# Optimization experiments

Hardware: AMD Instinct MI355X
Metric: run time of the kernel (lower is better)

Reference implementation:

```python
import jax, jax.numpy as jnp
import numpy as np

N, X_DIM, Z_DIM, H = 4096, 256, 128, 512
NUM_ACTIONS = 4
TEMPERATURE = 0.1


def _init_linear(key, fan_in, fan_out):
    kw, kb = jax.random.split(key)
    bound = 1.0 / np.sqrt(fan_in)
    W = jax.random.uniform(kw, (fan_in, fan_out), minval=-bound, maxval=bound, dtype=jnp.float32)
    b = jax.random.uniform(kb, (fan_out,), minval=-bound, maxval=bound, dtype=jnp.float32)
    return W, b


def setup_inputs() -> dict:
    key = jax.random.key(0)
    ks = jax.random.split(key, 9)
    s = jax.random.normal(ks[0], (N, X_DIM), dtype=jnp.float32)
    sp = jax.random.normal(ks[1], (N, X_DIM), dtype=jnp.float32)
    a = jax.random.randint(ks[2], (N,), 0, NUM_ACTIONS)
    a1h = jax.nn.one_hot(a, NUM_ACTIONS, dtype=jnp.float32)
    # phi: x_dim -> 512 -> 512 -> z_dim
    pW0, pb0 = _init_linear(ks[3], X_DIM, H)
    pW1, pb1 = _init_linear(ks[4], H, H)
    pW2, pb2 = _init_linear(ks[5], H, Z_DIM)
    # g: x_dim + 4 -> 512 -> 512 -> z_dim
    gW0, gb0 = _init_linear(ks[6], X_DIM + NUM_ACTIONS, H)
    gW1, gb1 = _init_linear(ks[7], H, H)
    gW2, gb2 = _init_linear(ks[8], H, Z_DIM)
    return {"s": s, "sp": sp, "a1h": a1h,
            "pW0": pW0, "pb0": pb0, "pW1": pW1, "pb1": pb1, "pW2": pW2, "pb2": pb2,
            "gW0": gW0, "gb0": gb0, "gW1": gW1, "gb1": gb1, "gW2": gW2, "gb2": gb2}


def _mlp(x, W0, b0, W1, b1, W2, b2):
    h = jax.nn.relu(x @ W0 + b0)
    h = jax.nn.relu(h @ W1 + b1)
    return h @ W2 + b2


def reference(s, sp, a1h, pW0, pb0, pW1, pb1, pW2, pb2, gW0, gb0, gW1, gb1, gW2, gb2):
    z = _mlp(s, pW0, pb0, pW1, pb1, pW2, pb2)                      # [N, D]
    zpos = _mlp(jnp.concatenate([sp, a1h], axis=-1), gW0, gb0, gW1, gb1, gW2, gb2)  # [N, D]
    # -||z_i - zpos_j||^2 / T via the GEMM trick (avoids the [N,N,D] diff tensor)
    sq_z = jnp.sum(z * z, axis=-1, keepdims=True)                  # [N, 1]
    sq_p = jnp.sum(zpos * zpos, axis=-1)                            # [N]
    logits = -(sq_z + sq_p[None, :] - 2.0 * z @ zpos.T) / TEMPERATURE  # [N, N]
    # cross-entropy with targets = arange(N): diagonal is the positive
    log_probs = jax.nn.log_softmax(logits, axis=-1)
    loss = -jnp.mean(jnp.diagonal(log_probs))
    return loss
```

## Files before the change

kernel.cpp:

```cpp
#include <hip/hip_runtime.h>
#include <math.h>

#define NR 4096
#define HD 512
#define NJR 16
#define INV_T 10.0f

typedef __attribute__((ext_vector_type(8))) short bf16x8;
typedef __attribute__((ext_vector_type(4))) short short4v;
typedef __attribute__((ext_vector_type(4))) float f32x4;

typedef const unsigned int __attribute__((address_space(1)))* gas_t;
typedef unsigned int __attribute__((address_space(3)))* las_t;

__device__ __forceinline__ unsigned short f2bf(float f) {
  union { float f; unsigned u; } v; v.f = f;
  unsigned r = v.u + 0x7fff + ((v.u >> 16) & 1);
  return (unsigned short)(r >> 16);
}
__device__ __forceinline__ float bf2f(unsigned short b) {
  union { unsigned u; float f; } v; v.u = ((unsigned)b) << 16;
  return v.f;
}


__device__ __forceinline__ void wt_unit(int local, int tid, const float* W,
                                        unsigned short* Wt, int N, int ksh) {
  const int idx8 = tid & 127;
  const int h = idx8 & 1, p = idx8 >> 1, hi = p >> 4, l15 = p & 15;
  int s0 = local * 2 + (tid >> 7);
  int rf = s0 >> ksh, ks = s0 & ((1 << ksh) - 1);
  int n = rf * 16 + l15, k0 = ks * 32 + hi * 4 + h * 16;
  short4v o = { (short)f2bf(W[(size_t)(k0 + 0) * N + n]),
                (short)f2bf(W[(size_t)(k0 + 1) * N + n]),
                (short)f2bf(W[(size_t)(k0 + 2) * N + n]),
                (short)f2bf(W[(size_t)(k0 + 3) * N + n]) };
  *(short4v*)((char*)Wt + (size_t)s0 * 1024 + idx8 * 8) = o;
}

__global__ __launch_bounds__(256) void prep(
    const float* __restrict__ s, const float* __restrict__ sp,
    const float* __restrict__ a1h,
    unsigned short* __restrict__ Sb, unsigned short* __restrict__ SPb,
    int* __restrict__ aidx, float* __restrict__ sqp,
    const float* __restrict__ pW0, unsigned short* __restrict__ pW0t,
    const float* __restrict__ gW0, unsigned short* __restrict__ gW0t,
    float* __restrict__ out) {
  const int tid = threadIdx.x;
  for (int u = blockIdx.x; u < 2320; u += 580) {
    if (u < 16) {
      int r = u * 256 + tid;
      int a = 0;
#pragma unroll
      for (int j = 0; j < 4; ++j) if (a1h[(size_t)r * 4 + j] > 0.5f) a = j;
      aidx[r] = a;
      sqp[r] = 0.f;
      if (u == 0 && tid == 0) out[0] = 0.f;
      continue;
    }
    if (u < 2064) {
      const int b = u;
      const float* src = (b < 1040) ? s : sp;
      unsigned short* dst = (b < 1040) ? Sb : SPb;
      int lb = (b < 1040) ? b - 16 : b - 1040;
      const int idx8 = tid & 127;
      const int h = idx8 & 1, p = idx8 >> 1, hi = p >> 4, l15 = p & 15;
      int s0 = lb * 2 + (tid >> 7);
      int rf = s0 >> 3, ks = s0 & 7;
      int row = rf * 16 + l15, c0 = ks * 32 + hi * 4 + h * 16;
      float4 v = *(const float4*)&src[(size_t)row * 256 + c0];
      short4v o = { (short)f2bf(v.x), (short)f2bf(v.y), (short)f2bf(v.z), (short)f2bf(v.w) };
      *(short4v*)((char*)dst + (size_t)s0 * 1024 + idx8 * 8) = o;
      continue;
    }
    int local = u - 2064;
    if (local < 128) wt_unit(local, tid, pW0, pW0t, 512, 3);
    else             wt_unit(local - 128, tid, gW0, gW0t, 512, 3);
  }
}

template <int BM, int K, bool RELU, bool GB, bool SQ, bool RIDERS>
__global__ __launch_bounds__(256) void gemm_p3(
    const unsigned short* __restrict__ A0, const unsigned short* __restrict__ A1,
    const unsigned short* __restrict__ W0, const unsigned short* __restrict__ W1,
    const float* __restrict__ b0, const float* __restrict__ b1,
    unsigned short* __restrict__ C0, unsigned short* __restrict__ C1,
    float* __restrict__ sqp, int N, int gx, int gy,
    const int* __restrict__ aidx, const float* __restrict__ gW0f,
    const float* __restrict__ rpW1, unsigned short* __restrict__ rpW1t,
    const float* __restrict__ rpW2, unsigned short* __restrict__ rpW2t,
    const float* __restrict__ rgW1, unsigned short* __restrict__ rgW1t,
    const float* __restrict__ rgW2, unsigned short* __restrict__ rgW2t) {
  const int tid = threadIdx.x;
  const int ngemm = gx * gy * 2;
  if (RIDERS && (int)blockIdx.x >= ngemm) {
    int local = blockIdx.x - ngemm;
    if (local < 256)      wt_unit(local, tid, rpW1, rpW1t, 512, 4);
    else if (local < 320) wt_unit(local - 256, tid, rpW2, rpW2t, 128, 4);
    else if (local < 576) wt_unit(local - 320, tid, rgW1, rgW1t, 512, 4);
    else                  wt_unit(local - 576, tid, rgW2, rgW2t, 128, 4);
    return;
  }
  constexpr int KS = K >> 5;
  constexpr int NSTEP = K >> 6;
  constexpr int ABYTES = BM * 128;
  constexpr int BBYTES = 8192;
  constexpr int NA = BM >> 5;
  constexpr int WM_FR = BM >> 5;
  constexpr int V = NA + 2;
  __shared__ char lds[3 * (ABYTES + BBYTES)];
  char* AsB = lds;
  char* BsB = lds + 3 * ABYTES;

  const int bid = blockIdx.x;
  const int bx = bid % gx, by = (bid / gx) % gy, z = bid / (gx * gy);
  const int lane = tid & 63, w = tid >> 6;
  const int wm = w >> 1, wn = w & 1;
  const char* Ab = (const char*)(z ? A1 : A0);
  const char* Wb = (const char*)(z ? W1 : W0);
  const float* bias = z ? b1 : b0;
  char* Cb = (char*)(z ? C1 : C0);
  const int bm = bx * BM, bn = by * 64;
  const int lane16 = lane * 16;

  auto stage = [&](int buf, int st) {
#pragma unroll
    for (int u = 0; u < NA; ++u) {
      const int sl = w * NA + u;
      const char* src = Ab + ((size_t)((bm >> 4) + (sl >> 1)) * KS + st * 2 + (sl & 1)) * 1024 + lane16;
      __builtin_amdgcn_global_load_lds((gas_t)src, (las_t)(AsB + buf * ABYTES + sl * 1024), 16, 0, 0);
    }
#pragma unroll
    for (int u = 0; u < 2; ++u) {
      const int sl = w * 2 + u;
      const char* src = Wb + ((size_t)((bn >> 4) + (sl >> 1)) * KS + st * 2 + (sl & 1)) * 1024 + lane16;
      __builtin_amdgcn_global_load_lds((gas_t)src, (las_t)(BsB + buf * BBYTES + sl * 1024), 16, 0, 0);
    }
  };

  f32x4 acc[WM_FR][2] = {};
  stage(0, 0);
  stage(1, 1);
#pragma unroll
  for (int st = 0; st < NSTEP; ++st) {
    const int buf = st % 3;
    if (st + 2 < NSTEP) {
      stage((st + 2) % 3, st + 2);
      if constexpr (V == 6) asm volatile("s_waitcnt vmcnt(12)" ::: "memory");
      else                  asm volatile("s_waitcnt vmcnt(8)" ::: "memory");
    } else if (st + 1 < NSTEP) {
      if constexpr (V == 6) asm volatile("s_waitcnt vmcnt(6)" ::: "memory");
      else                  asm volatile("s_waitcnt vmcnt(4)" ::: "memory");
    } else {
      asm volatile("s_waitcnt vmcnt(0)" ::: "memory");
    }
    __builtin_amdgcn_s_barrier();
#pragma unroll
    for (int kss = 0; kss < 2; ++kss) {
      bf16x8 af[WM_FR], bfv[2];
#pragma unroll
      for (int i = 0; i < WM_FR; ++i)
        af[i] = *(const bf16x8*)(AsB + buf * ABYTES + ((wm * WM_FR + i) * 2 + kss) * 1024 + lane16);
#pragma unroll
      for (int j = 0; j < 2; ++j)
        bfv[j] = *(const bf16x8*)(BsB + buf * BBYTES + ((wn * 2 + j) * 2 + kss) * 1024 + lane16);
#pragma unroll
      for (int i = 0; i < WM_FR; ++i)
#pragma unroll
        for (int j = 0; j < 2; ++j)
          acc[i][j] = __builtin_amdgcn_mfma_f32_16x16x32_bf16(bfv[j], af[i], acc[i][j], 0, 0, 0);
    }
    __builtin_amdgcn_s_barrier();
  }

  const int l15 = lane & 15, hi = lane >> 4;
  const int NS = N >> 5;
  const int row0 = bm + wm * (BM / 2);
  const int col0 = bn + wn * 32;
  float sq[WM_FR];
  int ar[WM_FR];
#pragma unroll
  for (int i = 0; i < WM_FR; ++i) { sq[i] = 0.f; ar[i] = 0; }
  if (GB && z == 1) {
#pragma unroll
    for (int i = 0; i < WM_FR; ++i) ar[i] = aidx[row0 + i * 16 + l15];
  }
  float4 bi0 = *(const float4*)&bias[col0 + hi * 4];
  float4 bi1 = *(const float4*)&bias[col0 + 16 + hi * 4];
#pragma unroll
  for (int i = 0; i < WM_FR; ++i) {
    const int rfC = (row0 >> 4) + i;
    float v[8] = { acc[i][0][0] + bi0.x, acc[i][0][1] + bi0.y,
                   acc[i][0][2] + bi0.z, acc[i][0][3] + bi0.w,
                   acc[i][1][0] + bi1.x, acc[i][1][1] + bi1.y,
                   acc[i][1][2] + bi1.z, acc[i][1][3] + bi1.w };
    if (GB && z == 1) {
      float4 g0 = *(const float4*)&gW0f[(size_t)(256 + ar[i]) * N + col0 + hi * 4];
      float4 g1 = *(const float4*)&gW0f[(size_t)(256 + ar[i]) * N + col0 + 16 + hi * 4];
      v[0] += g0.x; v[1] += g0.y; v[2] += g0.z; v[3] += g0.w;
      v[4] += g1.x; v[5] += g1.y; v[6] += g1.z; v[7] += g1.w;
    }
    bf16x8 r;
#pragma unroll
    for (int t = 0; t < 8; ++t) {
      float vv = RELU ? fmaxf(v[t], 0.f) : v[t];
      unsigned short cv = f2bf(vv);
      r[t] = (short)cv;
      if (SQ) { float vb = bf2f(cv); sq[i] += vb * vb; }
    }
    *(bf16x8*)(Cb + (size_t)(rfC * NS + (col0 >> 5)) * 1024 + lane16) = r;
  }
  if (SQ && z == 1) {
#pragma unroll
    for (int i = 0; i < WM_FR; ++i) {
      float t = sq[i];
      t += __shfl_xor(t, 16, 64);
      t += __shfl_xor(t, 32, 64);
      if (lane < 16) atomicAdd(&sqp[row0 + i * 16 + lane], t);
    }
  }
}

__global__ __launch_bounds__(256) void logits_fm(
    const unsigned short* __restrict__ Zb, const unsigned short* __restrict__ Zpb,
    const float* __restrict__ sqp, float* __restrict__ wm_,
    float* __restrict__ wsum, float* __restrict__ wdiag) {
  const int tid = threadIdx.x, lane = tid & 63, w = tid >> 6;
  const int l15 = lane & 15, hi = lane >> 4;
  const int i0 = blockIdx.x * 128, jr = blockIdx.y;
  const int row32 = i0 + w * 32;
  const int jbase = jr * 256;
  const int lane16 = lane * 16;
  const char* Zc = (const char*)Zb;
  const char* Pc = (const char*)Zpb;

  bf16x8 afr[2][4];
#pragma unroll
  for (int rf = 0; rf < 2; ++rf)
#pragma unroll
    for (int ks = 0; ks < 4; ++ks)
      afr[rf][ks] = *(const bf16x8*)(Zc + (size_t)(((row32 >> 4) + rf) * 4 + ks) * 1024 + lane16);

  float m[2] = {-INFINITY, -INFINITY}, sv[2] = {0.f, 0.f}, dd[2] = {0.f, 0.f};
  bool hasd[2] = {false, false};
  const int grow0 = row32 + l15, grow1 = row32 + 16 + l15;

#pragma unroll
  for (int g = 0; g < 4; ++g) {
    f32x4 acc[2][4] = {};
#pragma unroll
    for (int ks = 0; ks < 4; ++ks)
#pragma unroll
      for (int q = 0; q < 4; ++q) {
        bf16x8 bfv = *(const bf16x8*)(Pc + (size_t)(((jbase >> 4) + g * 4 + q) * 4 + ks) * 1024 + lane16);
        acc[0][q] = __builtin_amdgcn_mfma_f32_16x16x32_bf16(bfv, afr[0][ks], acc[0][q], 0, 0, 0);
        acc[1][q] = __builtin_amdgcn_mfma_f32_16x16x32_bf16(bfv, afr[1][ks], acc[1][q], 0, 0, 0);
      }
    f32x4 spq[4];
#pragma unroll
    for (int q = 0; q < 4; ++q)
      spq[q] = *(const f32x4*)&sqp[jbase + (g * 4 + q) * 16 + hi * 4];
#pragma unroll
    for (int rf = 0; rf < 2; ++rf) {
      const int grow = rf ? grow1 : grow0;
      float lv[16];
      float lmax = -INFINITY;
#pragma unroll
      for (int q = 0; q < 4; ++q)
#pragma unroll
        for (int e = 0; e < 4; ++e) {
          const int j = jbase + (g * 4 + q) * 16 + hi * 4 + e;
          float x = (2.f * acc[rf][q][e] - spq[q][e]) * INV_T;
          lv[q * 4 + e] = x;
          lmax = fmaxf(lmax, x);
          if (j == grow) { dd[rf] = x; hasd[rf] = true; }
        }
      float mn = fmaxf(m[rf], lmax);
      float sc = __expf(m[rf] - mn);
      float ls = 0.f;
#pragma unroll
      for (int t = 0; t < 16; ++t) ls += __expf(lv[t] - mn);
      sv[rf] = sv[rf] * sc + ls;
      m[rf] = mn;
    }
  }

#pragma unroll
  for (int rf = 0; rf < 2; ++rf) {
    const int grow = rf ? grow1 : grow0;
    float mm = m[rf], ss = sv[rf];
#pragma unroll
    for (int off = 16; off <= 32; off <<= 1) {
      float mo = __shfl_xor(mm, off, 64);
      float so = __shfl_xor(ss, off, 64);
      float mn = fmaxf(mm, mo);
      ss = ss * __expf(mm - mn) + so * __expf(mo - mn);
      mm = mn;
    }
    if (hi == 0) {
      wm_[(size_t)jr * NR + grow] = mm;
      wsum[(size_t)jr * NR + grow] = ss;
    }
    if (hasd[rf]) wdiag[grow] = dd[rf];
  }
}

__global__ __launch_bounds__(256) void finalize(const float* __restrict__ wm,
    const float* __restrict__ wsum, const float* __restrict__ wdiag,
    float* __restrict__ out) {
  int r = blockIdx.x * 256 + threadIdx.x;
  float mm = wm[r];
  float ss = wsum[r];
#pragma unroll
  for (int p = 1; p < NJR; ++p) {
    float mo = wm[(size_t)p * NR + r];
    float so = wsum[(size_t)p * NR + r];
    float mn = fmaxf(mm, mo);
    ss = ss * __expf(mm - mn) + so * __expf(mo - mn);
    mm = mn;
  }
  float loss_r = mm + logf(ss) - wdiag[r];
  float v = loss_r;
#pragma unroll
  for (int off = 32; off; off >>= 1) v += __shfl_xor(v, off, 64);
  __shared__ float partial[4];
  if ((threadIdx.x & 63) == 0) partial[threadIdx.x >> 6] = v;
  __syncthreads();
  if (threadIdx.x == 0)
    atomicAdd(out, (partial[0] + partial[1] + partial[2] + partial[3]) * (1.0f / (float)NR));
}

extern "C" void kernel_launch(void* const* d_in, const int* in_sizes, int n_in,
                              void* d_out, int out_size, void* d_ws, size_t ws_size,
                              hipStream_t stream) {
  const float* s   = (const float*)d_in[0];
  const float* sp  = (const float*)d_in[1];
  const float* a1h = (const float*)d_in[2];
  const float* pW0 = (const float*)d_in[3];
  const float* pb0 = (const float*)d_in[4];
  const float* pW1 = (const float*)d_in[5];
  const float* pb1 = (const float*)d_in[6];
  const float* pW2 = (const float*)d_in[7];
  const float* pb2 = (const float*)d_in[8];
  const float* gW0 = (const float*)d_in[9];
  const float* gb0 = (const float*)d_in[10];
  const float* gW1 = (const float*)d_in[11];
  const float* gb1 = (const float*)d_in[12];
  const float* gW2 = (const float*)d_in[13];
  const float* gb2 = (const float*)d_in[14];

  char* p = (char*)d_ws;
  unsigned short* Sb   = (unsigned short*)p; p += (size_t)NR * 256 * 2;
  unsigned short* SPb  = (unsigned short*)p; p += (size_t)NR * 256 * 2;
  unsigned short* H1   = (unsigned short*)p; p += (size_t)2 * NR * HD * 2;
  unsigned short* H2   = (unsigned short*)p; p += (size_t)2 * NR * HD * 2;
  unsigned short* Zall = (unsigned short*)p; p += (size_t)2 * NR * 128 * 2;
  unsigned short* pW0t = (unsigned short*)p; p += (size_t)256 * 512 * 2;
  unsigned short* pW1t = (unsigned short*)p; p += (size_t)512 * 512 * 2;
  unsigned short* pW2t = (unsigned short*)p; p += (size_t)512 * 128 * 2;
  unsigned short* gW0t = (unsigned short*)p; p += (size_t)256 * 512 * 2;
  unsigned short* gW1t = (unsigned short*)p; p += (size_t)512 * 512 * 2;
  unsigned short* gW2t = (unsigned short*)p; p += (size_t)512 * 128 * 2;
  float* sqp  = (float*)p; p += (size_t)NR * 4;
  float* wm   = (float*)p; p += (size_t)NJR * NR * 4;
  float* wsm  = (float*)p; p += (size_t)NJR * NR * 4;
  float* wdg  = (float*)p; p += (size_t)NR * 4;
  int*   aidx = (int*)p;  p += (size_t)NR * 4;

  unsigned short* H1g = H1 + (size_t)NR * HD;
  unsigned short* H2g = H2 + (size_t)NR * HD;
  unsigned short* Zb  = Zall;
  unsigned short* Zpb = Zall + (size_t)NR * 128;

  dim3 blk(256);
  prep<<<580, blk, 0, stream>>>(s, sp, a1h, Sb, SPb, aidx, sqp,
                                pW0, pW0t, gW0, gW0t, (float*)d_out);

  gemm_p3<128, 256, true, true, false, true><<<1152, blk, 0, stream>>>(
      Sb, SPb, pW0t, gW0t, pb0, gb0, H1, H1g, nullptr, 512, 32, 8, aidx, gW0,
      pW1, pW1t, pW2, pW2t, gW1, gW1t, gW2, gW2t);

  gemm_p3<128, 512, true, false, false, false><<<512, blk, 0, stream>>>(
      H1, H1g, pW1t, gW1t, pb1, gb1, H2, H2g, nullptr, 512, 32, 8, nullptr, nullptr,
      nullptr, nullptr, nullptr, nullptr, nullptr, nullptr, nullptr, nullptr);

  gemm_p3<64, 512, false, false, true, false><<<256, blk, 0, stream>>>(
      H2, H2g, pW2t, gW2t, pb2, gb2, Zb, Zpb, sqp, 128, 64, 2, nullptr, nullptr,
      nullptr, nullptr, nullptr, nullptr, nullptr, nullptr, nullptr, nullptr);

  logits_fm<<<dim3(32, NJR), blk, 0, stream>>>(Zb, Zpb, sqp, wm, wsm, wdg);
  finalize<<<NR / 256, blk, 0, stream>>>(wm, wsm, wdg, (float*)d_out);
}
```

Baseline: 46.18 us.

## Double-buffer zpos tiles in LDS and compute softmax in base-2 domain

New measurement: 47.87 us. 3.7% more time.

```diff
diff --git a/kernel.cpp b/kernel.cpp
--- a/kernel.cpp
+++ b/kernel.cpp
@@ -5,6 +5,12 @@
 #define HD 512
 #define NJR 16
 #define INV_T 10.0f
+#define CF  14.426950408889634f
+#define C2F 28.853900817779268f
+#define LN2 0.6931471805599453f
+
+#define EXP2F(x) __builtin_exp2f(x)
+#define LOG2F(x) __builtin_log2f(x)
 
 typedef __attribute__((ext_vector_type(8))) short bf16x8;
 typedef __attribute__((ext_vector_type(4))) short short4v;
@@ -225,6 +231,7 @@
     const unsigned short* __restrict__ Zb, const unsigned short* __restrict__ Zpb,
     const float* __restrict__ sqp, float* __restrict__ wm_,
     float* __restrict__ wsum, float* __restrict__ wdiag) {
+  __shared__ __align__(1024) char Ps[2][16384];
   const int tid = threadIdx.x, lane = tid & 63, w = tid >> 6;
   const int l15 = lane & 15, hi = lane >> 4;
   const int i0 = blockIdx.x * 128, jr = blockIdx.y;
@@ -233,7 +240,18 @@
   const int lane16 = lane * 16;
   const char* Zc = (const char*)Zb;
   const char* Pc = (const char*)Zpb;
-
+  const bool diagBlk = ((int)(blockIdx.x >> 1) == jr);
+
+  auto stageP = [&](int buf, int g) {
+#pragma unroll
+    for (int u = 0; u < 4; ++u) {
+      const int sl = w * 4 + u;
+      const char* src = Pc + (size_t)(((jbase >> 4) + g * 4 + (sl >> 2)) * 4 + (sl & 3)) * 1024 + lane16;
+      __builtin_amdgcn_global_load_lds((gas_t)src, (las_t)(Ps[buf] + sl * 1024), 16, 0, 0);
+    }
+  };
+
+  stageP(0, 0);
   bf16x8 afr[2][4];
 #pragma unroll
   for (int rf = 0; rf < 2; ++rf)
@@ -241,60 +259,81 @@
     for (int ks = 0; ks < 4; ++ks)
       afr[rf][ks] = *(const bf16x8*)(Zc + (size_t)(((row32 >> 4) + rf) * 4 + ks) * 1024 + lane16);
 
-  float m[2] = {-INFINITY, -INFINITY}, sv[2] = {0.f, 0.f}, dd[2] = {0.f, 0.f};
+  float m2[2] = {-INFINITY, -INFINITY}, sv[2] = {0.f, 0.f}, dd[2] = {0.f, 0.f};
   bool hasd[2] = {false, false};
   const int grow0 = row32 + l15, grow1 = row32 + 16 + l15;
 
-#pragma unroll
   for (int g = 0; g < 4; ++g) {
+    const int buf = g & 1;
+    if (g < 3) {
+      stageP(buf ^ 1, g + 1);
+      asm volatile("s_waitcnt vmcnt(4)" ::: "memory");
+    } else {
+      asm volatile("s_waitcnt vmcnt(0)" ::: "memory");
+    }
+    __builtin_amdgcn_s_barrier();
+
     f32x4 acc[2][4] = {};
 #pragma unroll
     for (int ks = 0; ks < 4; ++ks)
 #pragma unroll
       for (int q = 0; q < 4; ++q) {
-        bf16x8 bfv = *(const bf16x8*)(Pc + (size_t)(((jbase >> 4) + g * 4 + q) * 4 + ks) * 1024 + lane16);
+        bf16x8 bfv = *(const bf16x8*)(Ps[buf] + (q * 4 + ks) * 1024 + lane16);
         acc[0][q] = __builtin_amdgcn_mfma_f32_16x16x32_bf16(bfv, afr[0][ks], acc[0][q], 0, 0, 0);
         acc[1][q] = __builtin_amdgcn_mfma_f32_16x16x32_bf16(bfv, afr[1][ks], acc[1][q], 0, 0, 0);
       }
-    f32x4 spq[4];
-#pragma unroll
-    for (int q = 0; q < 4; ++q)
-      spq[q] = *(const f32x4*)&sqp[jbase + (g * 4 + q) * 16 + hi * 4];
+    __syncthreads();
+
+    f32x4 spC[4];
+#pragma unroll
+    for (int q = 0; q < 4; ++q) {
+      f32x4 t = *(const f32x4*)&sqp[jbase + (g * 4 + q) * 16 + hi * 4];
+      spC[q][0] = t[0] * CF; spC[q][1] = t[1] * CF;
+      spC[q][2] = t[2] * CF; spC[q][3] = t[3] * CF;
+    }
 #pragma unroll
     for (int rf = 0; rf < 2; ++rf) {
-      const int grow = rf ? grow1 : grow0;
       float lv[16];
       float lmax = -INFINITY;
 #pragma unroll
       for (int q = 0; q < 4; ++q)
 #pragma unroll
         for (int e = 0; e < 4; ++e) {
-          const int j = jbase + (g * 4 + q) * 16 + hi * 4 + e;
-          float x = (2.f * acc[rf][q][e] - spq[q][e]) * INV_T;
+          float x = fmaf(acc[rf][q][e], C2F, -spC[q][e]);
           lv[q * 4 + e] = x;
           lmax = fmaxf(lmax, x);
-          if (j == grow) { dd[rf] = x; hasd[rf] = true; }
         }
-      float mn = fmaxf(m[rf], lmax);
-      float sc = __expf(m[rf] - mn);
+      if (diagBlk) {
+        const int grow = rf ? grow1 : grow0;
+#pragma unroll
+        for (int q = 0; q < 4; ++q)
+#pragma unroll
+          for (int e = 0; e < 4; ++e)
+            if (jbase + (g * 4 + q) * 16 + hi * 4 + e == grow) {
+              dd[rf] = lv[q * 4 + e];
+              hasd[rf] = true;
+            }
+      }
+      float mn = fmaxf(m2[rf], lmax);
+      float sc = EXP2F(m2[rf] - mn);
       float ls = 0.f;
 #pragma unroll
-      for (int t = 0; t < 16; ++t) ls += __expf(lv[t] - mn);
+      for (int t = 0; t < 16; ++t) ls += EXP2F(lv[t] - mn);
       sv[rf] = sv[rf] * sc + ls;
-      m[rf] = mn;
+      m2[rf] = mn;
     }
   }
 
 #pragma unroll
   for (int rf = 0; rf < 2; ++rf) {
     const int grow = rf ? grow1 : grow0;
-    float mm = m[rf], ss = sv[rf];
+    float mm = m2[rf], ss = sv[rf];
 #pragma unroll
     for (int off = 16; off <= 32; off <<= 1) {
       float mo = __shfl_xor(mm, off, 64);
       float so = __shfl_xor(ss, off, 64);
       float mn = fmaxf(mm, mo);
-      ss = ss * __expf(mm - mn) + so * __expf(mo - mn);
+      ss = ss * EXP2F(mm - mn) + so * EXP2F(mo - mn);
       mm = mn;
     }
     if (hi == 0) {
@@ -316,10 +355,10 @@
     float mo = wm[(size_t)p * NR + r];
     float so = wsum[(size_t)p * NR + r];
     float mn = fmaxf(mm, mo);
-    ss = ss * __expf(mm - mn) + so * __expf(mo - mn);
+    ss = ss * EXP2F(mm - mn) + so * EXP2F(mo - mn);
     mm = mn;
   }
-  float loss_r = mm + logf(ss) - wdiag[r];
+  float loss_r = LN2 * (mm + LOG2F(ss) - wdiag[r]);
   float v = loss_r;
 #pragma unroll
   for (int off = 32; off; off >>= 1) v += __shfl_xor(v, off, 64);
```
